# Optimization experiments

Hardware: AMD Instinct MI355X
Metric: run time of the kernel (lower is better)

The kernel has to match this reference:

```python
import jax, jax.numpy as jnp
import numpy as np

B, S, D_IN, UNITS = 4, 4096, 512, 128

def setup_inputs() -> dict:
    key = jax.random.key(0)
    k_in, k_wq, k_wk, k_wv = jax.random.split(key, 4)
    scale = 1.0 / np.sqrt(D_IN)
    return {
        "inputs": jax.random.normal(k_in, (B, S, D_IN), dtype=jnp.float32),
        "Wq": jax.random.normal(k_wq, (D_IN, UNITS), dtype=jnp.float32) * scale,
        "bq": jnp.zeros((UNITS,), dtype=jnp.float32),
        "Wk": jax.random.normal(k_wk, (D_IN, UNITS), dtype=jnp.float32) * scale,
        "bk": jnp.zeros((UNITS,), dtype=jnp.float32),
        "Wv": jax.random.normal(k_wv, (D_IN, UNITS), dtype=jnp.float32) * scale,
        "bv": jnp.zeros((UNITS,), dtype=jnp.float32),
    }

def reference(inputs, Wq, bq, Wk, bk, Wv, bv):
    # Dense + ReLU projections (Keras Dense default has bias)
    q = jax.nn.relu(jnp.einsum('bsd,du->bsu', inputs, Wq) + bq)  # [B,S,U]
    k = jax.nn.relu(jnp.einsum('bsd,du->bsu', inputs, Wk) + bk)
    v = jax.nn.relu(jnp.einsum('bsd,du->bsu', inputs, Wv) + bv)
    # Raw (unscaled) attention: softmax(Q K^T) V
    scores = jnp.einsum('bsu,btu->bst', q, k)                    # [B,S,S]
    attn = jax.nn.softmax(scores, axis=-1)
    return jnp.einsum('bst,btu->bsu', attn, v)                   # [B,S,U]
```

## Files before the change

kernel.cpp:

```cpp
#include <hip/hip_runtime.h>
#include <stdint.h>

#define Bq 4
#define Sq 4096
#define DIN 512
#define Uq 128
#define Mq (Bq * Sq)
#define LOG2E 1.44269504f

typedef __attribute__((ext_vector_type(8))) _Float16 f16x8;
typedef __attribute__((ext_vector_type(4))) float f32x4;
typedef __attribute__((ext_vector_type(16))) float f32x16;
typedef unsigned short u16;

__device__ __forceinline__ u16 f2h(float f) {
  union { _Float16 h; u16 u; } v;
  v.h = (_Float16)f;
  return v.u;
}
__device__ __forceinline__ float h2f(u16 u) {
  union { u16 u; _Float16 h; } v;
  v.u = u;
  return (float)v.h;
}
__device__ __forceinline__ unsigned pk2(float a, float b) {
  return __builtin_bit_cast(unsigned, __builtin_amdgcn_cvt_pkrtz(a, b));
}
__device__ __forceinline__ void gl_lds16(const void* g, void* l) {
  __builtin_amdgcn_global_load_lds(
      (const __attribute__((address_space(1))) unsigned int*)g,
      (__attribute__((address_space(3))) unsigned int*)l, 16, 0, 0);
}
__device__ __forceinline__ float xmax32(float v) { return fmaxf(v, __shfl_xor(v, 32)); }
__device__ __forceinline__ float xsum32(float v) { return v + __shfl_xor(v, 32); }

#if defined(__has_builtin) && __has_builtin(__builtin_amdgcn_exp2f)
#define EXP2(x) __builtin_amdgcn_exp2f(x)
#else
#define EXP2(x) exp2f(x)
#endif

__global__ __launch_bounds__(256) void wt_kernel(const float* __restrict__ Wqp,
                                                 const float* __restrict__ Wkp,
                                                 const float* __restrict__ Wvp,
                                                 u16* __restrict__ wt) {
  int idx = blockIdx.x * 256 + threadIdx.x;
  int z = idx >> 16, r = idx & 65535;
  int n = r >> 9, k = r & 511;
  const float* W = (z == 0) ? Wqp : ((z == 1) ? Wkp : Wvp);
  wt[idx] = f2h(W[k * Uq + n]);
}

__global__ __launch_bounds__(256, 2) void proj_kernel(const float* __restrict__ X,
                                                      const u16* __restrict__ Wt,
                                                      const float* __restrict__ bqp,
                                                      const float* __restrict__ bkp,
                                                      const float* __restrict__ bvp,
                                                      u16* __restrict__ qkv) {
  const int mbase = blockIdx.x * 32;
  const int tid = threadIdx.x;
  const int wid = tid >> 6, lane = tid & 63;
  const int lo = lane & 15, g = lane >> 4;

  __shared__ __align__(16) u16 xt[32][40];

  f32x4 acc[2][6];
#pragma unroll
  for (int mg = 0; mg < 2; ++mg)
#pragma unroll
    for (int fi = 0; fi < 6; ++fi) acc[mg][fi] = (f32x4){0.f, 0.f, 0.f, 0.f};

  const int xrow = tid >> 2, xcc = (tid & 3) * 8;
  const float* xsrc = X + (size_t)(mbase + xrow) * DIN + xcc;
  float4 nv0, nv1;
  if (tid < 128) {
    nv0 = *(const float4*)xsrc;
    nv1 = *(const float4*)(xsrc + 4);
  }

  const u16* wp[6];
#pragma unroll
  for (int fi = 0; fi < 6; ++fi) {
    const int gf = 6 * wid + fi;
    const int R = (gf >> 3) * 128 + (gf & 7) * 16 + lo;
    wp[fi] = Wt + (size_t)R * 512 + 8 * g;
  }
  f16x8 bw[6];
#pragma unroll
  for (int fi = 0; fi < 6; ++fi) bw[fi] = *(const f16x8*)(wp[fi]);

  for (int step = 0; step < 16; ++step) {
    if (tid < 128) {
      union { u16 u[8]; uint4 v; } pk;
      pk.u[0] = f2h(nv0.x); pk.u[1] = f2h(nv0.y); pk.u[2] = f2h(nv0.z); pk.u[3] = f2h(nv0.w);
      pk.u[4] = f2h(nv1.x); pk.u[5] = f2h(nv1.y); pk.u[6] = f2h(nv1.z); pk.u[7] = f2h(nv1.w);
      *(uint4*)(&xt[xrow][xcc]) = pk.v;
    }
    __syncthreads();
    if (step < 15 && tid < 128) {
      const float* s2 = xsrc + (step + 1) * 32;
      nv0 = *(const float4*)s2;
      nv1 = *(const float4*)(s2 + 4);
    }
    f16x8 a0 = *(const f16x8*)(&xt[lo][8 * g]);
    f16x8 a1 = *(const f16x8*)(&xt[16 + lo][8 * g]);
#pragma unroll
    for (int fi = 0; fi < 6; ++fi) {
      acc[0][fi] = __builtin_amdgcn_mfma_f32_16x16x32_f16(a0, bw[fi], acc[0][fi], 0, 0, 0);
      acc[1][fi] = __builtin_amdgcn_mfma_f32_16x16x32_f16(a1, bw[fi], acc[1][fi], 0, 0, 0);
    }
    if (step < 15) {
#pragma unroll
      for (int fi = 0; fi < 6; ++fi)
        bw[fi] = *(const f16x8*)(wp[fi] + (step + 1) * 32);
    }
    __syncthreads();
  }

#pragma unroll
  for (int fi = 0; fi < 6; ++fi) {
    const int gf = 6 * wid + fi;
    const int z = gf >> 3, fl = gf & 7;
    const float* bias = (z == 0) ? bqp : ((z == 1) ? bkp : bvp);
    const float bb = bias[fl * 16 + lo];
    if (z < 2) {
      u16* dst = qkv + (size_t)z * Mq * Uq;
      const float qs = (z == 0) ? LOG2E : 1.0f;
#pragma unroll
      for (int mg = 0; mg < 2; ++mg)
#pragma unroll
        for (int r = 0; r < 4; ++r) {
          const int m = mbase + 16 * mg + 4 * g + r;
          dst[(size_t)m * Uq + fl * 16 + lo] = f2h(fmaxf(acc[mg][fi][r] + bb, 0.f) * qs);
        }
    } else {
      u16* vT = qkv + (size_t)2 * Mq * Uq;
      const int n = fl * 16 + lo;
#pragma unroll
      for (int mg = 0; mg < 2; ++mg) {
        const int m0 = mbase + 16 * mg + 4 * g;
        const int bb_ = m0 >> 12, s0 = m0 & (Sq - 1);
        ushort4 pv = make_ushort4(f2h(fmaxf(acc[mg][fi][0] + bb, 0.f)),
                                  f2h(fmaxf(acc[mg][fi][1] + bb, 0.f)),
                                  f2h(fmaxf(acc[mg][fi][2] + bb, 0.f)),
                                  f2h(fmaxf(acc[mg][fi][3] + bb, 0.f)));
        *(ushort4*)(vT + (size_t)bb_ * Uq * Sq + (size_t)n * Sq + s0) = pv;
      }
    }
  }
}

__global__ __launch_bounds__(256, 2) void attn_kernel(const u16* __restrict__ qkv,
                                                      u16* __restrict__ op,
                                                      float2* __restrict__ mlp,
                                                      int kvlen) {
  const int nb = gridDim.x;
  const int bid = blockIdx.x;
  const int xcd = bid & 7, idx = bid >> 3;
  const int b = xcd >> 1;
  const int within = (xcd & 1) * (nb >> 3) + idx;
  const int split = within >> 5, qblk = within & 31;
  const int kv0 = split * kvlen;
  const int kvrem = Sq - kv0;
  const int nit = ((kvrem < kvlen) ? kvrem : kvlen) >> 6;

  const int tid = threadIdx.x;
  const int wid = tid >> 6, lane = tid & 63;
  const int l32 = lane & 31, hi = lane >> 5;

  const u16* kbase = qkv + (size_t)Mq * Uq + (size_t)b * Sq * Uq;
  const u16* vbase = qkv + (size_t)2 * Mq * Uq + (size_t)b * Uq * Sq;

  __shared__ __align__(16) unsigned char kt[16384];
  __shared__ __align__(16) unsigned char vt[16384];
  __shared__ float smx[4][32];

  const int s4 = lane >> 4, j16 = lane & 15;
  const char* kg = (const char*)kbase + (size_t)(kv0 + 16 * wid) * 256 + 16 * lane;
  const int kwo0 = (16 * wid + 0 + s4) * 256 + ((j16 ^ ((0 + s4) & 7)) << 4);
  const int kwo1 = (16 * wid + 4 + s4) * 256 + ((j16 ^ ((4 + s4) & 7)) << 4);
  const int kwo2 = (16 * wid + 8 + s4) * 256 + ((j16 ^ ((8 + s4) & 7)) << 4);
  const int kwo3 = (16 * wid + 12 + s4) * 256 + ((j16 ^ ((12 + s4) & 7)) << 4);

  const int s8 = lane >> 3, j8 = lane & 7;
  const int vo = s8 * 8192 + ((j8 ^ s8) << 4);
  const char* vgp = (const char*)vbase + (size_t)kv0 * 2 + (size_t)wid * 262144 + vo;
  char* const vl = (char*)vt + wid * 4096;

#define VSTAGE() do {                       \
    gl_lds16(vgp,          vl);             \
    gl_lds16(vgp + 65536,  vl + 1024);      \
    gl_lds16(vgp + 131072, vl + 2048);      \
    gl_lds16(vgp + 196608, vl + 3072);      \
  } while (0)
#define KLOAD() do {                        \
    ka0 = *(const uint4*)(kg + 0);          \
    ka1 = *(const uint4*)(kg + 1024);       \
    ka2 = *(const uint4*)(kg + 2048);       \
    ka3 = *(const uint4*)(kg + 3072);       \
    kg += 16384;                            \
  } while (0)
#define KWRITE() do {                       \
    *(uint4*)(&kt[kwo0]) = ka0;             \
    *(uint4*)(&kt[kwo1]) = ka1;             \
    *(uint4*)(&kt[kwo2]) = ka2;             \
    *(uint4*)(&kt[kwo3]) = ka3;             \
  } while (0)

  const int qrow = b * Sq + qblk * 128 + wid * 32 + l32;
  f16x8 qf[8];
#pragma unroll
  for (int ks = 0; ks < 8; ++ks)
    qf[ks] = *(const f16x8*)(qkv + (size_t)qrow * Uq + 16 * ks + 8 * hi);

  f32x16 acc4[4];
#pragma unroll
  for (int f = 0; f < 4; ++f) acc4[f] = (f32x16){};
  float m_run = -1e30f, l_run = 0.f;
  float* const smxw = &smx[wid][0];

  const int q7 = l32 & 7;

  uint4 ka0, ka1, ka2, ka3;

  VSTAGE();
  KLOAD();
  asm volatile("s_waitcnt vmcnt(0)" ::: "memory");
  KWRITE();
  if (nit > 1) KLOAD();
  asm volatile("s_waitcnt lgkmcnt(0)" ::: "memory");
  __builtin_amdgcn_sched_barrier(0);
  __builtin_amdgcn_s_barrier();
  __builtin_amdgcn_sched_barrier(0);

  for (int it = 0; it < nit; ++it) {
    f32x16 sf0 = (f32x16){}, sf1 = (f32x16){};
    __builtin_amdgcn_s_setprio(1);
#pragma unroll
    for (int ks = 0; ks < 8; ++ks) {
      const int co = ((2 * ks + hi) ^ q7) << 4;
      f16x8 a0 = *(const f16x8*)(&kt[l32 * 256 + co]);
      f16x8 a1 = *(const f16x8*)(&kt[(32 + l32) * 256 + co]);
      sf0 = __builtin_amdgcn_mfma_f32_32x32x16_f16(a0, qf[ks], sf0, 0, 0, 0);
      sf1 = __builtin_amdgcn_mfma_f32_32x32x16_f16(a1, qf[ks], sf1, 0, 0, 0);
    }
    __builtin_amdgcn_s_setprio(0);

    float t8[8];
#pragma unroll
    for (int i = 0; i < 8; ++i)
      t8[i] = fmaxf(fmaxf(sf0[i], sf0[i + 8]), fmaxf(sf1[i], sf1[i + 8]));
#pragma unroll
    for (int i = 0; i < 4; ++i) t8[i] = fmaxf(t8[i], t8[i + 4]);
    float tmax = fmaxf(fmaxf(t8[0], t8[1]), fmaxf(t8[2], t8[3]));
    tmax = xmax32(tmax);

    if (__any(tmax > m_run + 8.f)) {
      const float m_new = fmaxf(m_run, tmax);
      const float sc = EXP2(m_run - m_new);
      if (lane < 32) smxw[l32] = sc;
#pragma unroll
      for (int r = 0; r < 16; ++r) {
        const float scr = smxw[(r & 3) + 8 * (r >> 2) + 4 * hi];
#pragma unroll
        for (int f = 0; f < 4; ++f) acc4[f][r] *= scr;
      }
      l_run *= sc;
      m_run = m_new;
    }

    float psum = 0.f;
    unsigned Ap[2][4], Bp[2][4];
#pragma unroll
    for (int ks2 = 0; ks2 < 2; ++ks2) {
#pragma unroll
      for (int m = 0; m < 4; ++m) {
        const float s0v = ks2 ? sf1[4 * m + 0] : sf0[4 * m + 0];
        const float s1v = ks2 ? sf1[4 * m + 1] : sf0[4 * m + 1];
        const float s2v = ks2 ? sf1[4 * m + 2] : sf0[4 * m + 2];
        const float s3v = ks2 ? sf1[4 * m + 3] : sf0[4 * m + 3];
        const float p0 = EXP2(s0v - m_run), p1 = EXP2(s1v - m_run);
        const float p2 = EXP2(s2v - m_run), p3 = EXP2(s3v - m_run);
        psum += (p0 + p1) + (p2 + p3);
        Ap[ks2][m] = pk2(p0, p1);
        Bp[ks2][m] = pk2(p2, p3);
      }
    }
    l_run += xsum32(psum);

    f16x8 pa[4];
#pragma unroll
    for (int ks2 = 0; ks2 < 2; ++ks2)
#pragma unroll
      for (int kk = 0; kk < 2; ++kk) {
        const unsigned sa = hi ? Ap[ks2][2 * kk] : Ap[ks2][2 * kk + 1];
        const unsigned sb = hi ? Bp[ks2][2 * kk] : Bp[ks2][2 * kk + 1];
        const unsigned xa = (unsigned)__shfl_xor((int)sa, 32);
        const unsigned xb = (unsigned)__shfl_xor((int)sb, 32);
        const unsigned oa = hi ? Ap[ks2][2 * kk + 1] : Ap[ks2][2 * kk];
        const unsigned ob = hi ? Bp[ks2][2 * kk + 1] : Bp[ks2][2 * kk];
        union { unsigned u[4]; f16x8 v; } w;
        w.u[0] = hi ? xa : oa;
        w.u[1] = hi ? xb : ob;
        w.u[2] = hi ? oa : xa;
        w.u[3] = hi ? ob : xb;
        pa[2 * ks2 + kk] = w.v;
      }

    if (it + 1 < nit) asm volatile("s_waitcnt vmcnt(4)" ::: "memory");
    else              asm volatile("s_waitcnt vmcnt(0)" ::: "memory");
    __builtin_amdgcn_sched_barrier(0);
    __builtin_amdgcn_s_barrier();
    __builtin_amdgcn_sched_barrier(0);

    __builtin_amdgcn_s_setprio(1);
#pragma unroll
    for (int ks = 0; ks < 4; ++ks) {
#pragma unroll
      for (int f = 0; f < 4; ++f) {
        const int d = 32 * f + l32;
        f16x8 bv = *(const f16x8*)(&vt[d * 128 + (((2 * ks + hi) ^ q7) << 4)]);
        acc4[f] = __builtin_amdgcn_mfma_f32_32x32x16_f16(pa[ks], bv, acc4[f], 0, 0, 0);
      }
    }
    __builtin_amdgcn_s_setprio(0);

    if (it + 1 < nit) KWRITE();
    asm volatile("s_waitcnt lgkmcnt(0)" ::: "memory");
    __builtin_amdgcn_sched_barrier(0);
    __builtin_amdgcn_s_barrier();
    __builtin_amdgcn_sched_barrier(0);

    if (it + 1 < nit) {
      vgp += 128;
      VSTAGE();
      if (it + 2 < nit) KLOAD();
    }
  }
#undef VSTAGE
#undef KLOAD
#undef KWRITE

  if (lane < 32) smxw[l32] = 1.f / l_run;
  const size_t rb = (size_t)split * Mq + (size_t)b * Sq + qblk * 128 + wid * 32;
  if (lane < 32) mlp[rb + lane] = make_float2(m_run, l_run);
  u16* od = op + rb * Uq;
#pragma unroll
  for (int f = 0; f < 4; ++f)
#pragma unroll
    for (int r = 0; r < 16; ++r) {
      const int qr = (r & 3) + 8 * (r >> 2) + 4 * hi;
      od[(size_t)qr * Uq + 32 * f + l32] = f2h(acc4[f][r] * smxw[qr]);
    }
}

__global__ __launch_bounds__(256) void combine_kernel(const u16* __restrict__ op,
                                                      const float2* __restrict__ mlp,
                                                      float* __restrict__ out,
                                                      int nsplit) {
  const int idx = blockIdx.x * 256 + threadIdx.x;
  const int q = idx >> 5, nq = idx & 31;
  float M = -1e30f;
  for (int s = 0; s < nsplit; ++s) M = fmaxf(M, mlp[(size_t)s * Mq + q].x);
  float L = 0.f;
  float ox = 0.f, oy = 0.f, oz = 0.f, ow = 0.f;
  for (int s = 0; s < nsplit; ++s) {
    const float2 ml = mlp[(size_t)s * Mq + q];
    const float w = EXP2(ml.x - M) * ml.y;
    L += w;
    const ushort4 v = *(const ushort4*)(op + ((size_t)s * Mq + q) * Uq + nq * 4);
    ox += w * h2f(v.x); oy += w * h2f(v.y); oz += w * h2f(v.z); ow += w * h2f(v.w);
  }
  const float inv = 1.f / L;
  *(float4*)(out + (size_t)q * Uq + nq * 4) = make_float4(ox * inv, oy * inv, oz * inv, ow * inv);
}

extern "C" void kernel_launch(void* const* d_in, const int* in_sizes, int n_in,
                              void* d_out, int out_size, void* d_ws, size_t ws_size,
                              hipStream_t stream) {
  const float* X   = (const float*)d_in[0];
  const float* Wqp = (const float*)d_in[1];
  const float* bqp = (const float*)d_in[2];
  const float* Wkp = (const float*)d_in[3];
  const float* bkp = (const float*)d_in[4];
  const float* Wvp = (const float*)d_in[5];
  const float* bvp = (const float*)d_in[6];
  float* out = (float*)d_out;

  u16* qkv = (u16*)d_ws;
  u16* wt  = qkv + (size_t)3 * Mq * Uq;
  u16* op  = wt + 3 * 65536;

  const size_t base = (size_t)12976128;
  const size_t per  = (size_t)(Mq * Uq * 2 + Mq * 8);
  int nsplit = 4;
  if (ws_size < base + 4 * per) nsplit = 2;
  if (ws_size < base + 2 * per) nsplit = 1;
  float2* mlp = (float2*)(op + (size_t)nsplit * Mq * Uq);
  const int kvlen = Sq / nsplit;

  wt_kernel<<<768, 256, 0, stream>>>(Wqp, Wkp, Wvp, wt);
  proj_kernel<<<Mq / 32, 256, 0, stream>>>(X, wt, bqp, bkp, bvp, qkv);
  attn_kernel<<<128 * nsplit, 256, 0, stream>>>(qkv, op, mlp, kvlen);
  combine_kernel<<<(Mq * 32) / 256, 256, 0, stream>>>(op, mlp, out, nsplit);
}
```

Measured before the change: 86.16 us.

## Double-buffer K and V tiles in LDS to drop a barrier per iteration

Splits the K and V shared-memory tiles into two ping-pong buffers. The next tile's V async copy and K register-to-LDS write now go into the alternate buffer at the start of each iteration, and the loop keeps a single barrier at the end instead of two. The aim is to overlap global loads and LDS writes with both MFMA phases and to cut synchronisation. In exchange it doubles LDS use to 64KB per block, which may lower occupancy, and the K write now has to wait for the previous KLOAD's vmcnt to drain early in the iteration.

```diff
diff --git a/kernel.cpp b/kernel.cpp
--- a/kernel.cpp
+++ b/kernel.cpp
@@ -171,8 +171,8 @@
   const u16* kbase = qkv + (size_t)Mq * Uq + (size_t)b * Sq * Uq;
   const u16* vbase = qkv + (size_t)2 * Mq * Uq + (size_t)b * Uq * Sq;
 
-  __shared__ __align__(16) unsigned char kt[16384];
-  __shared__ __align__(16) unsigned char vt[16384];
+  __shared__ __align__(16) unsigned char kt[2][16384];
+  __shared__ __align__(16) unsigned char vt[2][16384];
   __shared__ float smx[4][32];
 
   const int s4 = lane >> 4, j16 = lane & 15;
@@ -185,13 +185,13 @@
   const int s8 = lane >> 3, j8 = lane & 7;
   const int vo = s8 * 8192 + ((j8 ^ s8) << 4);
   const char* vgp = (const char*)vbase + (size_t)kv0 * 2 + (size_t)wid * 262144 + vo;
-  char* const vl = (char*)vt + wid * 4096;
-
-#define VSTAGE() do {                       \
-    gl_lds16(vgp,          vl);             \
-    gl_lds16(vgp + 65536,  vl + 1024);      \
-    gl_lds16(vgp + 131072, vl + 2048);      \
-    gl_lds16(vgp + 196608, vl + 3072);      \
+
+#define VSTAGE(B) do {                                   \
+    char* vl_ = (char*)&vt[B][wid * 4096];               \
+    gl_lds16(vgp,          vl_);                         \
+    gl_lds16(vgp + 65536,  vl_ + 1024);                  \
+    gl_lds16(vgp + 131072, vl_ + 2048);                  \
+    gl_lds16(vgp + 196608, vl_ + 3072);                  \
   } while (0)
 #define KLOAD() do {                        \
     ka0 = *(const uint4*)(kg + 0);          \
@@ -200,11 +200,11 @@
     ka3 = *(const uint4*)(kg + 3072);       \
     kg += 16384;                            \
   } while (0)
-#define KWRITE() do {                       \
-    *(uint4*)(&kt[kwo0]) = ka0;             \
-    *(uint4*)(&kt[kwo1]) = ka1;             \
-    *(uint4*)(&kt[kwo2]) = ka2;             \
-    *(uint4*)(&kt[kwo3]) = ka3;             \
+#define KWRITE(B) do {                      \
+    *(uint4*)(&kt[B][kwo0]) = ka0;          \
+    *(uint4*)(&kt[B][kwo1]) = ka1;          \
+    *(uint4*)(&kt[B][kwo2]) = ka2;          \
+    *(uint4*)(&kt[B][kwo3]) = ka3;          \
   } while (0)
 
   const int qrow = b * Sq + qblk * 128 + wid * 32 + l32;
@@ -223,10 +223,10 @@
 
   uint4 ka0, ka1, ka2, ka3;
 
-  VSTAGE();
+  VSTAGE(0);
   KLOAD();
   asm volatile("s_waitcnt vmcnt(0)" ::: "memory");
-  KWRITE();
+  KWRITE(0);
   if (nit > 1) KLOAD();
   asm volatile("s_waitcnt lgkmcnt(0)" ::: "memory");
   __builtin_amdgcn_sched_barrier(0);
@@ -234,13 +234,22 @@
   __builtin_amdgcn_sched_barrier(0);
 
   for (int it = 0; it < nit; ++it) {
+    const int p = it & 1;
+
+    if (it + 1 < nit) {
+      vgp += 128;
+      VSTAGE(p ^ 1);
+      KWRITE(p ^ 1);
+      if (it + 2 < nit) KLOAD();
+    }
+
     f32x16 sf0 = (f32x16){}, sf1 = (f32x16){};
     __builtin_amdgcn_s_setprio(1);
 #pragma unroll
     for (int ks = 0; ks < 8; ++ks) {
       const int co = ((2 * ks + hi) ^ q7) << 4;
-      f16x8 a0 = *(const f16x8*)(&kt[l32 * 256 + co]);
-      f16x8 a1 = *(const f16x8*)(&kt[(32 + l32) * 256 + co]);
+      f16x8 a0 = *(const f16x8*)(&kt[p][l32 * 256 + co]);
+      f16x8 a1 = *(const f16x8*)(&kt[p][(32 + l32) * 256 + co]);
       sf0 = __builtin_amdgcn_mfma_f32_32x32x16_f16(a0, qf[ks], sf0, 0, 0, 0);
       sf1 = __builtin_amdgcn_mfma_f32_32x32x16_f16(a1, qf[ks], sf1, 0, 0, 0);
     }
@@ -307,35 +316,24 @@
         pa[2 * ks2 + kk] = w.v;
       }
 
-    if (it + 1 < nit) asm volatile("s_waitcnt vmcnt(4)" ::: "memory");
-    else              asm volatile("s_waitcnt vmcnt(0)" ::: "memory");
+    __builtin_amdgcn_s_setprio(1);
+#pragma unroll
+    for (int ks = 0; ks < 4; ++ks) {
+#pragma unroll
+      for (int f = 0; f < 4; ++f) {
+        const int d = 32 * f + l32;
+        f16x8 bv = *(const f16x8*)(&vt[p][d * 128 + (((2 * ks + hi) ^ q7) << 4)]);
+        acc4[f] = __builtin_amdgcn_mfma_f32_32x32x16_f16(pa[ks], bv, acc4[f], 0, 0, 0);
+      }
+    }
+    __builtin_amdgcn_s_setprio(0);
+
+    asm volatile("s_waitcnt lgkmcnt(0)" ::: "memory");
+    if (it + 2 < nit)      asm volatile("s_waitcnt vmcnt(4)" ::: "memory");
+    else if (it + 1 < nit) asm volatile("s_waitcnt vmcnt(0)" ::: "memory");
     __builtin_amdgcn_sched_barrier(0);
     __builtin_amdgcn_s_barrier();
     __builtin_amdgcn_sched_barrier(0);
-
-    __builtin_amdgcn_s_setprio(1);
-#pragma unroll
-    for (int ks = 0; ks < 4; ++ks) {
-#pragma unroll
-      for (int f = 0; f < 4; ++f) {
-        const int d = 32 * f + l32;
-        f16x8 bv = *(const f16x8*)(&vt[d * 128 + (((2 * ks + hi) ^ q7) << 4)]);
-        acc4[f] = __builtin_amdgcn_mfma_f32_32x32x16_f16(pa[ks], bv, acc4[f], 0, 0, 0);
-      }
-    }
-    __builtin_amdgcn_s_setprio(0);
-
-    if (it + 1 < nit) KWRITE();
-    asm volatile("s_waitcnt lgkmcnt(0)" ::: "memory");
-    __builtin_amdgcn_sched_barrier(0);
-    __builtin_amdgcn_s_barrier();
-    __builtin_amdgcn_sched_barrier(0);
-
-    if (it + 1 < nit) {
-      vgp += 128;
-      VSTAGE();
-      if (it + 2 < nit) KLOAD();
-    }
   }
 #undef VSTAGE
 #undef KLOAD
```

Result: no change. 87.43 us (+1.5%).
